# Performance work log

Hardware: AMD Instinct MI355X
Metric: run time of the kernel (lower is better)

## Reference

```python
import jax, jax.numpy as jnp
import numpy as np

P = 16       # n_partitions
E = 512      # entity_dim
H = 512      # hidden_dim
N = 8192     # number of entities in the batch


def setup_inputs() -> dict:
    key = jax.random.key(0)
    ks = jax.random.split(key, 7)
    s_in = 1.0 / np.sqrt(E)
    s_h = 1.0 / np.sqrt(H)
    return {
        "e_embedding": jax.random.normal(ks[0], (N, E), dtype=jnp.float32),
        # stacked weights for the P independent SimpleMLPs (fused as batched GEMMs)
        "W0": jax.random.uniform(ks[1], (P, E, H), jnp.float32, -s_in, s_in),
        "b0": jax.random.uniform(ks[2], (P, H), jnp.float32, -s_in, s_in),
        "W1": jax.random.uniform(ks[3], (P, H, H), jnp.float32, -s_h, s_h),
        "b1": jax.random.uniform(ks[4], (P, H), jnp.float32, -s_h, s_h),
        "W2": jax.random.uniform(ks[5], (P, H, 1), jnp.float32, -s_h, s_h),
        "b2": jax.random.uniform(ks[6], (P, 1), jnp.float32, -s_h, s_h),
    }


def reference(e_embedding, W0, b0, W1, b1, W2, b2):
    # Each partition p runs SimpleMLP_p(e_embedding); fused as batched einsums.
    h = jax.nn.relu(jnp.einsum("ne,peh->pnh", e_embedding, W0) + b0[:, None, :])  # [P,N,H]
    h = jax.nn.relu(jnp.einsum("pnh,phk->pnk", h, W1) + b1[:, None, :])           # [P,N,H]
    out = jnp.einsum("pnh,pho->pno", h, W2) + b2[:, None, :]                      # [P,N,1]
    out = jax.nn.sigmoid(out)  # regularizer: fuzzy membership in [0,1]
    # torch.stack(...).squeeze().T  ->  [P,N] -> [N,P]
    return jnp.squeeze(out, axis=-1).T
```

## Files before the change

kernel.cpp:

```cpp
#include <hip/hip_runtime.h>
#include <stdint.h>

typedef _Float16 f16;
typedef _Float16 f16x8 __attribute__((ext_vector_type(8)));
typedef float floatx4 __attribute__((ext_vector_type(4)));
typedef unsigned short u16;

#define PDIM 16

__device__ __forceinline__ floatx4 mfma_16x16x32(f16x8 a, f16x8 b, floatx4 c) {
  return __builtin_amdgcn_mfma_f32_16x16x32_f16(a, b, c, 0, 0, 0);
}

__device__ __forceinline__ void stage16(const f16* g, f16* lds_base) {
  __builtin_amdgcn_global_load_lds(
      (const __attribute__((address_space(1))) void*)g,
      (__attribute__((address_space(3))) void*)lds_base, 16, 0, 0);
}

#define WAITVM4() asm volatile("s_waitcnt vmcnt(4)" ::: "memory")
#define WAITVM2() asm volatile("s_waitcnt vmcnt(2)" ::: "memory")
#define WAITVM0() asm volatile("s_waitcnt vmcnt(0)" ::: "memory")
#define BAR()     asm volatile("s_barrier" ::: "memory")
#define LGKM0()   asm volatile("s_waitcnt lgkmcnt(0)" ::: "memory")
#define SCHEDFENCE() __builtin_amdgcn_sched_barrier(0)
#define PRIO1() __builtin_amdgcn_s_setprio(1)
#define PRIO0() __builtin_amdgcn_s_setprio(0)


__device__ __forceinline__ void decode_block2(int b, int nwg, int& p, int& ht,
                                              int& nt) {
  const int NT = nwg >> 5;
  if ((NT & 7) == 0) {
    const int x  = b & 7;
    const int u  = b >> 3;
    const int i  = u & 31;
    const int cg = u >> 5;
    ht = i & 1;
    const int pl  = (i >> 1) & 1;
    const int ntl = i >> 2;
    p  = x * 2 + pl;
    nt = cg * 8 + ntl;
  } else {
    p  = b & 15;
    ht = (b >> 4) & 1;
    nt = b >> 5;
  }
}

__global__ __launch_bounds__(256) void kprep(const float* __restrict__ emb,
                                             const float* __restrict__ W0,
                                             const float* __restrict__ W1,
                                             const float* __restrict__ b0,
                                             const float* __restrict__ b1,
                                             const float* __restrict__ W2,
                                             const float* __restrict__ b2,
                                             f16* __restrict__ embB,
                                             f16* __restrict__ W0T,
                                             f16* __restrict__ W1T,
                                             float* __restrict__ smallF,
                                             int n8, int nConvBlk) {
  __shared__ unsigned int tile[16384];
  const int b = blockIdx.x;
  const int t = threadIdx.x;
  if (b < 256) {
    const int m  = b >> 7;
    const int p  = (b >> 3) & 15;
    const int tc = b & 7;
    const int hb = tc * 64;
    const float* src = (m ? W1 : W0) + ((size_t)p << 18);
    f16*         dst = (m ? W1T : W0T) + ((size_t)p << 18);
    const int er = t >> 2;
    const int hq = t & 3;
#pragma unroll
    for (int j = 0; j < 8; ++j) {
      const int e   = er + j * 64;
      const int swz = (e >> 3) & 31;
      const float* rp = src + (size_t)e * 512 + hb;
#pragma unroll
      for (int i = 0; i < 4; ++i) {
        const int hc = hq * 4 + i * 16;
        float4 v = *(const float4*)(rp + hc);
        union { f16 h2[2]; unsigned int u; } w0, w1;
        w0.h2[0] = (f16)v.x; w0.h2[1] = (f16)v.y;
        w1.h2[0] = (f16)v.z; w1.h2[1] = (f16)v.w;
        const int hp = hc >> 1;
        tile[e * 32 + (hp ^ swz)]       = w0.u;
        tile[e * 32 + ((hp + 1) ^ swz)] = w1.u;
      }
    }
    __syncthreads();
    const int w = t >> 6, l = t & 63;
#pragma unroll
    for (int P = 0; P < 16; ++P) {
      const int hl  = P * 4 + w;
      const int hp  = hl >> 1;
      const int sub = hl & 1;
      union { u16 uu[8]; uint4 v; } o;
#pragma unroll
      for (int j = 0; j < 8; ++j) {
        const int e = l * 8 + j;
        const unsigned int word = tile[e * 32 + (hp ^ ((e >> 3) & 31))];
        o.uu[j] = (u16)(sub ? (word >> 16) : (word & 0xffffu));
      }
      *(uint4*)(dst + (size_t)(hb + hl) * 512 + l * 8) = o.v;
    }
  } else if (b < 256 + nConvBlk) {
    const int i = (b - 256) * 256 + t;
    if (i < n8) {
      const float4* s = (const float4*)emb;
      float4 a = s[i * 2], bb = s[i * 2 + 1];
      union { f16 h[8]; uint4 v; } o;
      o.h[0] = (f16)a.x;  o.h[1] = (f16)a.y;  o.h[2] = (f16)a.z;  o.h[3] = (f16)a.w;
      o.h[4] = (f16)bb.x; o.h[5] = (f16)bb.y; o.h[6] = (f16)bb.z; o.h[7] = (f16)bb.w;
      *(uint4*)(embB + (size_t)i * 8) = o.v;
    }
  } else {
    const int j = (b - 256 - nConvBlk) * 256 + t;
    if (j < 24592) {
      const float* src;
      int off;
      if (j < 8192)       { src = b0; off = j; }
      else if (j < 16384) { src = b1; off = j - 8192; }
      else if (j < 24576) { src = W2; off = j - 16384; }
      else                { src = b2; off = j - 24576; }
      smallF[j] = src[off];
    }
  }
}

__device__ __forceinline__ void stageU(const f16* M, int h, int tt, f16* buf,
                                       int w, int srow8, int kg8) {
  stage16(M + (size_t)(h * 128 + w * 8 + srow8) * 512 + tt * 64 + kg8,
          buf + (w * 8) * 64);
  stage16(M + (size_t)(h * 128 + 64 + w * 8 + srow8) * 512 + tt * 64 + kg8,
          buf + (64 + w * 8) * 64);
}

__device__ __forceinline__ void gemm_core4(const f16* __restrict__ Arow,
                                           const f16* __restrict__ Brow,
                                           f16* smem, floatx4 (*acc)[2][2][4],
                                           int w, int lane) {
  const int q   = lane >> 4;
  const int mm  = lane & 15;
  const int mm7 = mm & 7;
  const int qwr = (w & 3) * 32;
  const int qwc = (w >> 2) * 64;
  const int srow8 = lane >> 3;
  const int kg8   = (((lane & 7) ^ ((lane >> 3) & 7)) * 8);

  stageU(Arow, 0, 0, smem + 0 * 8192, w, srow8, kg8);
  stageU(Brow, 0, 0, smem + 32768 + 0 * 8192, w, srow8, kg8);
  stageU(Brow, 1, 0, smem + 32768 + 1 * 8192, w, srow8, kg8);
  stageU(Arow, 1, 0, smem + 1 * 8192, w, srow8, kg8);

  f16x8 af[2][2], bv[4][2];

  for (int t = 0; t < 8; ++t) {
    const int cb = t & 1;
    const f16* Ah0 = smem + (cb * 2 + 0) * 8192;
    const f16* Ah1 = smem + (cb * 2 + 1) * 8192;
    const f16* Bh0 = smem + 32768 + (cb * 2 + 0) * 8192;
    const f16* Bh1 = smem + 32768 + (cb * 2 + 1) * 8192;
    const int nb = cb ^ 1;
    f16* nAh0 = smem + (nb * 2 + 0) * 8192;
    f16* nAh1 = smem + (nb * 2 + 1) * 8192;
    f16* nBh0 = smem + 32768 + (nb * 2 + 0) * 8192;
    f16* nBh1 = smem + 32768 + (nb * 2 + 1) * 8192;

    WAITVM4();
    BAR();
#pragma unroll
    for (int rt = 0; rt < 2; ++rt)
#pragma unroll
      for (int ks = 0; ks < 2; ++ks)
        af[rt][ks] = *(const f16x8*)&Ah0[(qwr + rt * 16 + mm) * 64 +
                                         (((ks * 4 + q) ^ mm7)) * 8];
#pragma unroll
    for (int ct = 0; ct < 4; ++ct)
#pragma unroll
      for (int ks = 0; ks < 2; ++ks)
        bv[ct][ks] = *(const f16x8*)&Bh0[(qwc + ct * 16 + mm) * 64 +
                                         (((ks * 4 + q) ^ mm7)) * 8];
    if (t < 7) stageU(Arow, 0, t + 1, nAh0, w, srow8, kg8);
    LGKM0();
    PRIO1();
#pragma unroll
    for (int rt = 0; rt < 2; ++rt)
#pragma unroll
      for (int ct = 0; ct < 4; ++ct)
#pragma unroll
        for (int ks = 0; ks < 2; ++ks)
          acc[0][0][rt][ct] = mfma_16x16x32(af[rt][ks], bv[ct][ks],
                                            acc[0][0][rt][ct]);
    PRIO0();
    SCHEDFENCE();

    if (t < 7) { WAITVM4(); } else { WAITVM2(); }
    BAR();
#pragma unroll
    for (int ct = 0; ct < 4; ++ct)
#pragma unroll
      for (int ks = 0; ks < 2; ++ks)
        bv[ct][ks] = *(const f16x8*)&Bh1[(qwc + ct * 16 + mm) * 64 +
                                         (((ks * 4 + q) ^ mm7)) * 8];
    if (t < 7) stageU(Brow, 0, t + 1, nBh0, w, srow8, kg8);
    LGKM0();
    PRIO1();
#pragma unroll
    for (int rt = 0; rt < 2; ++rt)
#pragma unroll
      for (int ct = 0; ct < 4; ++ct)
#pragma unroll
        for (int ks = 0; ks < 2; ++ks)
          acc[0][1][rt][ct] = mfma_16x16x32(af[rt][ks], bv[ct][ks],
                                            acc[0][1][rt][ct]);
    PRIO0();
    SCHEDFENCE();

    if (t < 7) { WAITVM4(); } else { WAITVM0(); }
    BAR();
#pragma unroll
    for (int rt = 0; rt < 2; ++rt)
#pragma unroll
      for (int ks = 0; ks < 2; ++ks)
        af[rt][ks] = *(const f16x8*)&Ah1[(qwr + rt * 16 + mm) * 64 +
                                         (((ks * 4 + q) ^ mm7)) * 8];
    if (t < 7) stageU(Brow, 1, t + 1, nBh1, w, srow8, kg8);
    LGKM0();
    PRIO1();
#pragma unroll
    for (int rt = 0; rt < 2; ++rt)
#pragma unroll
      for (int ct = 0; ct < 4; ++ct)
#pragma unroll
        for (int ks = 0; ks < 2; ++ks)
          acc[1][1][rt][ct] = mfma_16x16x32(af[rt][ks], bv[ct][ks],
                                            acc[1][1][rt][ct]);
    PRIO0();
    SCHEDFENCE();

    BAR();
#pragma unroll
    for (int ct = 0; ct < 4; ++ct)
#pragma unroll
      for (int ks = 0; ks < 2; ++ks)
        bv[ct][ks] = *(const f16x8*)&Bh0[(qwc + ct * 16 + mm) * 64 +
                                         (((ks * 4 + q) ^ mm7)) * 8];
    if (t < 7) stageU(Arow, 1, t + 1, nAh1, w, srow8, kg8);
    LGKM0();
    PRIO1();
#pragma unroll
    for (int rt = 0; rt < 2; ++rt)
#pragma unroll
      for (int ct = 0; ct < 4; ++ct)
#pragma unroll
        for (int ks = 0; ks < 2; ++ks)
          acc[1][0][rt][ct] = mfma_16x16x32(af[rt][ks], bv[ct][ks],
                                            acc[1][0][rt][ct]);
    PRIO0();
    SCHEDFENCE();
  }
}

__device__ __forceinline__ void gemm_core2(const f16* __restrict__ Arow,
                                           const f16* __restrict__ Brow,
                                           f16* smem, floatx4 (*acc)[2][2][4],
                                           int w, int lane) {
  const int q   = lane >> 4;
  const int mm  = lane & 15;
  const int mm7 = mm & 7;
  const int qwr = (w & 3) * 32;
  const int qwc = (w >> 2) * 64;
  const int srow8 = lane >> 3;
  const int kg8   = (((lane & 7) ^ ((lane >> 3) & 7)) * 8);

  stageU(Arow, 0, 0, smem + 0 * 8192, w, srow8, kg8);
  stageU(Brow, 0, 0, smem + 32768 + 0 * 8192, w, srow8, kg8);
  stageU(Brow, 1, 0, smem + 32768 + 1 * 8192, w, srow8, kg8);
  stageU(Arow, 1, 0, smem + 1 * 8192, w, srow8, kg8);

  f16x8 af[2][2], bv[4][2];

  for (int t = 0; t < 8; ++t) {
    const int cb = t & 1;
    const f16* Ah0 = smem + (cb * 2 + 0) * 8192;
    const f16* Ah1 = smem + (cb * 2 + 1) * 8192;
    const f16* Bh0 = smem + 32768 + (cb * 2 + 0) * 8192;
    const f16* Bh1 = smem + 32768 + (cb * 2 + 1) * 8192;
    const int nb = cb ^ 1;
    f16* nAh0 = smem + (nb * 2 + 0) * 8192;
    f16* nAh1 = smem + (nb * 2 + 1) * 8192;
    f16* nBh0 = smem + 32768 + (nb * 2 + 0) * 8192;
    f16* nBh1 = smem + 32768 + (nb * 2 + 1) * 8192;

    WAITVM4();
    SCHEDFENCE();
    BAR();
#pragma unroll
    for (int rt = 0; rt < 2; ++rt)
#pragma unroll
      for (int ks = 0; ks < 2; ++ks)
        af[rt][ks] = *(const f16x8*)&Ah0[(qwr + rt * 16 + mm) * 64 +
                                         (((ks * 4 + q) ^ mm7)) * 8];
#pragma unroll
    for (int ct = 0; ct < 4; ++ct)
#pragma unroll
      for (int ks = 0; ks < 2; ++ks)
        bv[ct][ks] = *(const f16x8*)&Bh0[(qwc + ct * 16 + mm) * 64 +
                                         (((ks * 4 + q) ^ mm7)) * 8];
    if (t < 7) {
      stageU(Arow, 0, t + 1, nAh0, w, srow8, kg8);
      stageU(Brow, 0, t + 1, nBh0, w, srow8, kg8);
    }
    PRIO1();
#pragma unroll
    for (int rt = 0; rt < 2; ++rt)
#pragma unroll
      for (int ct = 0; ct < 4; ++ct)
#pragma unroll
        for (int ks = 0; ks < 2; ++ks)
          acc[0][0][rt][ct] = mfma_16x16x32(af[rt][ks], bv[ct][ks],
                                            acc[0][0][rt][ct]);
    PRIO0();

    if (t < 7) { WAITVM4(); } else { WAITVM0(); }
    SCHEDFENCE();
    BAR();
#pragma unroll
    for (int ct = 0; ct < 4; ++ct)
#pragma unroll
      for (int ks = 0; ks < 2; ++ks)
        bv[ct][ks] = *(const f16x8*)&Bh1[(qwc + ct * 16 + mm) * 64 +
                                         (((ks * 4 + q) ^ mm7)) * 8];
    if (t < 7) {
      stageU(Brow, 1, t + 1, nBh1, w, srow8, kg8);
      stageU(Arow, 1, t + 1, nAh1, w, srow8, kg8);
    }
    PRIO1();
#pragma unroll
    for (int rt = 0; rt < 2; ++rt)
#pragma unroll
      for (int ct = 0; ct < 4; ++ct)
#pragma unroll
        for (int ks = 0; ks < 2; ++ks)
          acc[0][1][rt][ct] = mfma_16x16x32(af[rt][ks], bv[ct][ks],
                                            acc[0][1][rt][ct]);
    PRIO0();
#pragma unroll
    for (int rt = 0; rt < 2; ++rt)
#pragma unroll
      for (int ks = 0; ks < 2; ++ks)
        af[rt][ks] = *(const f16x8*)&Ah1[(qwr + rt * 16 + mm) * 64 +
                                         (((ks * 4 + q) ^ mm7)) * 8];
    PRIO1();
#pragma unroll
    for (int rt = 0; rt < 2; ++rt)
#pragma unroll
      for (int ct = 0; ct < 4; ++ct)
#pragma unroll
        for (int ks = 0; ks < 2; ++ks)
          acc[1][1][rt][ct] = mfma_16x16x32(af[rt][ks], bv[ct][ks],
                                            acc[1][1][rt][ct]);
    PRIO0();
#pragma unroll
    for (int ct = 0; ct < 4; ++ct)
#pragma unroll
      for (int ks = 0; ks < 2; ++ks)
        bv[ct][ks] = *(const f16x8*)&Bh0[(qwc + ct * 16 + mm) * 64 +
                                         (((ks * 4 + q) ^ mm7)) * 8];
    PRIO1();
#pragma unroll
    for (int rt = 0; rt < 2; ++rt)
#pragma unroll
      for (int ct = 0; ct < 4; ++ct)
#pragma unroll
        for (int ks = 0; ks < 2; ++ks)
          acc[1][0][rt][ct] = mfma_16x16x32(af[rt][ks], bv[ct][ks],
                                            acc[1][0][rt][ct]);
    PRIO0();
    SCHEDFENCE();
  }
}

__global__ __launch_bounds__(512) void kgemm1(const f16* __restrict__ emb,
                                              const f16* __restrict__ W0T,
                                              const float* __restrict__ small,
                                              f16* __restrict__ h0,
                                              int Nc) {
  __shared__ f16 smem[65536];
  const int b  = blockIdx.x;
  const int p  = b & 15;
  const int ht = (b >> 4) & 1;
  const int nt = b >> 5;
  const int n0 = nt * 256;
  const int hc0 = ht * 256;
  const int tid = threadIdx.x;
  const int w = tid >> 6;
  const int lane = tid & 63;
  const int q = lane >> 4;
  const int mm = lane & 15;

  const f16* Arow = emb + (size_t)n0 * 512;
  const f16* Brow = W0T + ((size_t)p << 18) + (size_t)hc0 * 512;

  floatx4 acc[2][2][2][4];
#pragma unroll
  for (int i = 0; i < 2; ++i)
#pragma unroll
    for (int j = 0; j < 2; ++j)
#pragma unroll
      for (int k = 0; k < 2; ++k)
#pragma unroll
        for (int l = 0; l < 4; ++l) acc[i][j][k][l] = floatx4{0.f, 0.f, 0.f, 0.f};

  gemm_core4(Arow, Brow, smem, acc, w, lane);

  __syncthreads();
  f16* Cst = smem;
#pragma unroll
  for (int P = 0; P < 4; ++P) {
    if (((w & 3) >> 1) == (P & 1)) {
#pragma unroll
      for (int qn = 0; qn < 2; ++qn)
#pragma unroll
        for (int ct = 0; ct < 4; ++ct) {
          const int col = qn * 128 + (w >> 2) * 64 + ct * 16 + mm;
          const float bvv = small[p * 512 + hc0 + col];
#pragma unroll
          for (int rt = 0; rt < 2; ++rt)
#pragma unroll
            for (int r = 0; r < 4; ++r) {
              float v = acc[P >> 1][qn][rt][ct][r] + bvv;
              v = v > 0.f ? v : 0.f;
              Cst[((w & 1) * 32 + rt * 16 + q * 4 + r) * 264 + col] = (f16)v;
            }
        }
    }
    __syncthreads();
#pragma unroll
    for (int k = 0; k < 4; ++k) {
      const int idx = tid + k * 512;
      const int row = idx >> 5;
      const int ch  = idx & 31;
      uint4 v = *(const uint4*)&Cst[row * 264 + ch * 8];
      *(uint4*)&h0[((size_t)p * Nc + n0 + P * 64 + row) * 512 + hc0 + ch * 8] = v;
    }
    if (P < 3) __syncthreads();
  }
}

__global__ __launch_bounds__(512) void kgemm2(const f16* __restrict__ h0,
                                              const f16* __restrict__ W1T,
                                              const float* __restrict__ small,
                                              float* __restrict__ pacc,
                                              int Nc) {
  __shared__ f16 smem[65536];
  __shared__ float oacc[256];
  int p, ht, nt;
  decode_block2(blockIdx.x, gridDim.x, p, ht, nt);
  const int n0 = nt * 256;
  const int hc0 = ht * 256;
  const int tid = threadIdx.x;
  const int w = tid >> 6;
  const int lane = tid & 63;
  const int q = lane >> 4;
  const int mm = lane & 15;
  if (tid < 256) oacc[tid] = 0.f;

  const f16* Arow = h0 + ((size_t)p * Nc + n0) * 512;
  const f16* Brow = W1T + ((size_t)p << 18) + (size_t)hc0 * 512;

  floatx4 acc[2][2][2][4];
#pragma unroll
  for (int i = 0; i < 2; ++i)
#pragma unroll
    for (int j = 0; j < 2; ++j)
#pragma unroll
      for (int k = 0; k < 2; ++k)
#pragma unroll
        for (int l = 0; l < 4; ++l) acc[i][j][k][l] = floatx4{0.f, 0.f, 0.f, 0.f};

  gemm_core2(Arow, Brow, smem, acc, w, lane);

  __syncthreads();
#pragma unroll
  for (int qm = 0; qm < 2; ++qm) {
    float pd[2][4];
#pragma unroll
    for (int rt = 0; rt < 2; ++rt)
#pragma unroll
      for (int r = 0; r < 4; ++r) pd[rt][r] = 0.f;
#pragma unroll
    for (int qn = 0; qn < 2; ++qn)
#pragma unroll
      for (int ct = 0; ct < 4; ++ct) {
        const int col = hc0 + qn * 128 + (w >> 2) * 64 + ct * 16 + mm;
        const float b1v = small[8192 + p * 512 + col];
        const float w2v = small[16384 + p * 512 + col];
#pragma unroll
        for (int rt = 0; rt < 2; ++rt)
#pragma unroll
          for (int r = 0; r < 4; ++r) {
            float v = acc[qm][qn][rt][ct][r] + b1v;
            v = v > 0.f ? v : 0.f;
            pd[rt][r] += v * w2v;
          }
      }
#pragma unroll
    for (int rt = 0; rt < 2; ++rt)
#pragma unroll
      for (int r = 0; r < 4; ++r) {
        float v = pd[rt][r];
        v += __shfl_xor(v, 1, 16);
        v += __shfl_xor(v, 2, 16);
        v += __shfl_xor(v, 4, 16);
        v += __shfl_xor(v, 8, 16);
        if (mm == 0)
          atomicAdd(&oacc[qm * 128 + (w & 3) * 32 + rt * 16 + q * 4 + r], v);
      }
  }
  __syncthreads();
  if (tid < 256)
    pacc[(size_t)(p * 2 + ht) * Nc + n0 + tid] = oacc[tid];
}

__global__ __launch_bounds__(256) void kfin(const float* __restrict__ pacc,
                                            const float* __restrict__ small,
                                            float* __restrict__ out, int Nc) {
  const int idx = blockIdx.x * 256 + threadIdx.x;
  if (idx >= Nc * 16) return;
  const int n = idx >> 4;
  const int p = idx & 15;
  float v = small[24576 + p];
#pragma unroll
  for (int ht = 0; ht < 2; ++ht) v += pacc[(size_t)(p * 2 + ht) * Nc + n];
  out[(size_t)n * 16 + p] = 1.f / (1.f + expf(-v));
}

__global__ __launch_bounds__(64) void knaive(const float* __restrict__ emb,
                                             const float* __restrict__ W0,
                                             const float* __restrict__ b0,
                                             const float* __restrict__ W1,
                                             const float* __restrict__ b1,
                                             const float* __restrict__ W2,
                                             const float* __restrict__ b2,
                                             float* __restrict__ out) {
  const int n = blockIdx.x >> 4;
  const int p = blockIdx.x & 15;
  __shared__ float h0s[512];
  __shared__ float h1s[512];
  const size_t wb = (size_t)p << 18;
  const int t = threadIdx.x;
  for (int h = t; h < 512; h += 64) {
    float a = 0.f;
    for (int e = 0; e < 512; ++e)
      a += emb[(size_t)n * 512 + e] * W0[wb + (size_t)e * 512 + h];
    a += b0[p * 512 + h];
    h0s[h] = a > 0.f ? a : 0.f;
  }
  __syncthreads();
  for (int k = t; k < 512; k += 64) {
    float a = 0.f;
    for (int hh = 0; hh < 512; ++hh)
      a += h0s[hh] * W1[wb + (size_t)hh * 512 + k];
    a += b1[p * 512 + k];
    h1s[k] = a > 0.f ? a : 0.f;
  }
  __syncthreads();
  float s = 0.f;
  for (int k = t; k < 512; k += 64) s += h1s[k] * W2[p * 512 + k];
  for (int off = 32; off; off >>= 1) s += __shfl_down(s, off, 64);
  if (t == 0)
    out[(size_t)n * 16 + p] = 1.f / (1.f + expf(-(s + b2[p])));
}

extern "C" void kernel_launch(void* const* d_in, const int* in_sizes, int n_in,
                              void* d_out, int out_size, void* d_ws, size_t ws_size,
                              hipStream_t stream) {
  (void)n_in; (void)out_size;
  const float* emb = (const float*)d_in[0];
  const float* W0  = (const float*)d_in[1];
  const float* b0  = (const float*)d_in[2];
  const float* W1  = (const float*)d_in[3];
  const float* b1  = (const float*)d_in[4];
  const float* W2  = (const float*)d_in[5];
  const float* b2  = (const float*)d_in[6];
  float* out = (float*)d_out;

  const int N = in_sizes[0] / 512;

  char* ws = (char*)d_ws;
  f16*   W0T    = (f16*)ws;
  f16*   W1T    = (f16*)(ws + (8ll << 20));
  float* smallF = (float*)(ws + (16ll << 20));
  float* pacc   = (float*)(ws + (16ll << 20) + 131072);
  f16*   embB   = (f16*)(ws + (16ll << 20) + 131072 + (size_t)N * 256);
  f16*   h0     = (f16*)(ws + (16ll << 20) + 131072 + (size_t)N * 256 +
                         (size_t)N * 1024);
  const long long fixed = (16ll << 20) + 131072 + (long long)N * 256 +
                          (long long)N * 1024;
  long long avail = (long long)ws_size - fixed;
  long long rows = avail > 0 ? avail / (16 * 512 * 2) : 0;
  int Nc = (int)((rows / 256) * 256);
  if (Nc > N) Nc = N;

  if (Nc < 256 || (N % 256) != 0) {
    knaive<<<dim3(N * PDIM), dim3(64), 0, stream>>>(emb, W0, b0, W1, b1, W2,
                                                    b2, out);
    return;
  }

  const int n8 = N * 512 / 8;
  const int nConvBlk = (n8 + 255) / 256;
  kprep<<<dim3(256 + nConvBlk + 97), dim3(256), 0, stream>>>(
      emb, W0, W1, b0, b1, W2, b2, embB, W0T, W1T, smallF, n8, nConvBlk);

  for (int noff = 0; noff < N; noff += Nc) {
    const int cur = (N - noff < Nc) ? (N - noff) : Nc;
    kgemm1<<<dim3(32 * (cur / 256)), dim3(512), 0, stream>>>(
        embB + (size_t)noff * 512, W0T, smallF, h0, cur);
    kgemm2<<<dim3(32 * (cur / 256)), dim3(512), 0, stream>>>(
        h0, W1T, smallF, pacc, cur);
    kfin<<<dim3((cur * 16 + 255) / 256), dim3(256), 0, stream>>>(
        pacc, smallF, out + (size_t)noff * 16, cur);
  }
}
```

Measured before the change: 245.5 us.

## Fuse final sigmoid into kgemm2 by looping both hidden halves per block

kgemm2 now handles both 256-column halves of the hidden dimension in a sequential loop inside one block, accumulating the W2 dot product in shared memory, then adds b2, applies the sigmoid and writes the output directly. This removes the kfin kernel launch and the pacc round trip through global memory. In exchange the kgemm2 grid is halved (16 blocks per 256-row tile instead of 32), so there is less parallelism and each block runs twice as long. The A tile is re-staged for each half.

```diff
diff --git a/kernel.cpp b/kernel.cpp
--- a/kernel.cpp
+++ b/kernel.cpp
@@ -27,26 +27,6 @@
 #define PRIO1() __builtin_amdgcn_s_setprio(1)
 #define PRIO0() __builtin_amdgcn_s_setprio(0)
 
-
-__device__ __forceinline__ void decode_block2(int b, int nwg, int& p, int& ht,
-                                              int& nt) {
-  const int NT = nwg >> 5;
-  if ((NT & 7) == 0) {
-    const int x  = b & 7;
-    const int u  = b >> 3;
-    const int i  = u & 31;
-    const int cg = u >> 5;
-    ht = i & 1;
-    const int pl  = (i >> 1) & 1;
-    const int ntl = i >> 2;
-    p  = x * 2 + pl;
-    nt = cg * 8 + ntl;
-  } else {
-    p  = b & 15;
-    ht = (b >> 4) & 1;
-    nt = b >> 5;
-  }
-}
 
 __global__ __launch_bounds__(256) void kprep(const float* __restrict__ emb,
                                              const float* __restrict__ W0,
@@ -263,126 +243,6 @@
   }
 }
 
-__device__ __forceinline__ void gemm_core2(const f16* __restrict__ Arow,
-                                           const f16* __restrict__ Brow,
-                                           f16* smem, floatx4 (*acc)[2][2][4],
-                                           int w, int lane) {
-  const int q   = lane >> 4;
-  const int mm  = lane & 15;
-  const int mm7 = mm & 7;
-  const int qwr = (w & 3) * 32;
-  const int qwc = (w >> 2) * 64;
-  const int srow8 = lane >> 3;
-  const int kg8   = (((lane & 7) ^ ((lane >> 3) & 7)) * 8);
-
-  stageU(Arow, 0, 0, smem + 0 * 8192, w, srow8, kg8);
-  stageU(Brow, 0, 0, smem + 32768 + 0 * 8192, w, srow8, kg8);
-  stageU(Brow, 1, 0, smem + 32768 + 1 * 8192, w, srow8, kg8);
-  stageU(Arow, 1, 0, smem + 1 * 8192, w, srow8, kg8);
-
-  f16x8 af[2][2], bv[4][2];
-
-  for (int t = 0; t < 8; ++t) {
-    const int cb = t & 1;
-    const f16* Ah0 = smem + (cb * 2 + 0) * 8192;
-    const f16* Ah1 = smem + (cb * 2 + 1) * 8192;
-    const f16* Bh0 = smem + 32768 + (cb * 2 + 0) * 8192;
-    const f16* Bh1 = smem + 32768 + (cb * 2 + 1) * 8192;
-    const int nb = cb ^ 1;
-    f16* nAh0 = smem + (nb * 2 + 0) * 8192;
-    f16* nAh1 = smem + (nb * 2 + 1) * 8192;
-    f16* nBh0 = smem + 32768 + (nb * 2 + 0) * 8192;
-    f16* nBh1 = smem + 32768 + (nb * 2 + 1) * 8192;
-
-    WAITVM4();
-    SCHEDFENCE();
-    BAR();
-#pragma unroll
-    for (int rt = 0; rt < 2; ++rt)
-#pragma unroll
-      for (int ks = 0; ks < 2; ++ks)
-        af[rt][ks] = *(const f16x8*)&Ah0[(qwr + rt * 16 + mm) * 64 +
-                                         (((ks * 4 + q) ^ mm7)) * 8];
-#pragma unroll
-    for (int ct = 0; ct < 4; ++ct)
-#pragma unroll
-      for (int ks = 0; ks < 2; ++ks)
-        bv[ct][ks] = *(const f16x8*)&Bh0[(qwc + ct * 16 + mm) * 64 +
-                                         (((ks * 4 + q) ^ mm7)) * 8];
-    if (t < 7) {
-      stageU(Arow, 0, t + 1, nAh0, w, srow8, kg8);
-      stageU(Brow, 0, t + 1, nBh0, w, srow8, kg8);
-    }
-    PRIO1();
-#pragma unroll
-    for (int rt = 0; rt < 2; ++rt)
-#pragma unroll
-      for (int ct = 0; ct < 4; ++ct)
-#pragma unroll
-        for (int ks = 0; ks < 2; ++ks)
-          acc[0][0][rt][ct] = mfma_16x16x32(af[rt][ks], bv[ct][ks],
-                                            acc[0][0][rt][ct]);
-    PRIO0();
-
-    if (t < 7) { WAITVM4(); } else { WAITVM0(); }
-    SCHEDFENCE();
-    BAR();
-#pragma unroll
-    for (int ct = 0; ct < 4; ++ct)
-#pragma unroll
-      for (int ks = 0; ks < 2; ++ks)
-        bv[ct][ks] = *(const f16x8*)&Bh1[(qwc + ct * 16 + mm) * 64 +
-                                         (((ks * 4 + q) ^ mm7)) * 8];
-    if (t < 7) {
-      stageU(Brow, 1, t + 1, nBh1, w, srow8, kg8);
-      stageU(Arow, 1, t + 1, nAh1, w, srow8, kg8);
-    }
-    PRIO1();
-#pragma unroll
-    for (int rt = 0; rt < 2; ++rt)
-#pragma unroll
-      for (int ct = 0; ct < 4; ++ct)
-#pragma unroll
-        for (int ks = 0; ks < 2; ++ks)
-          acc[0][1][rt][ct] = mfma_16x16x32(af[rt][ks], bv[ct][ks],
-                                            acc[0][1][rt][ct]);
-    PRIO0();
-#pragma unroll
-    for (int rt = 0; rt < 2; ++rt)
-#pragma unroll
-      for (int ks = 0; ks < 2; ++ks)
-        af[rt][ks] = *(const f16x8*)&Ah1[(qwr + rt * 16 + mm) * 64 +
-                                         (((ks * 4 + q) ^ mm7)) * 8];
-    PRIO1();
-#pragma unroll
-    for (int rt = 0; rt < 2; ++rt)
-#pragma unroll
-      for (int ct = 0; ct < 4; ++ct)
-#pragma unroll
-        for (int ks = 0; ks < 2; ++ks)
-          acc[1][1][rt][ct] = mfma_16x16x32(af[rt][ks], bv[ct][ks],
-                                            acc[1][1][rt][ct]);
-    PRIO0();
-#pragma unroll
-    for (int ct = 0; ct < 4; ++ct)
-#pragma unroll
-      for (int ks = 0; ks < 2; ++ks)
-        bv[ct][ks] = *(const f16x8*)&Bh0[(qwc + ct * 16 + mm) * 64 +
-                                         (((ks * 4 + q) ^ mm7)) * 8];
-    PRIO1();
-#pragma unroll
-    for (int rt = 0; rt < 2; ++rt)
-#pragma unroll
-      for (int ct = 0; ct < 4; ++ct)
-#pragma unroll
-        for (int ks = 0; ks < 2; ++ks)
-          acc[1][0][rt][ct] = mfma_16x16x32(af[rt][ks], bv[ct][ks],
-                                            acc[1][0][rt][ct]);
-    PRIO0();
-    SCHEDFENCE();
-  }
-}
-
 __global__ __launch_bounds__(512) void kgemm1(const f16* __restrict__ emb,
                                               const f16* __restrict__ W0T,
                                               const float* __restrict__ small,
@@ -450,17 +310,153 @@
   }
 }
 
+__device__ __forceinline__ void gemm_core2(const f16* __restrict__ Arow,
+                                           const f16* __restrict__ Brow,
+                                           f16* smem, floatx4 (*acc)[2][2][4],
+                                           int w, int lane) {
+  const int q   = lane >> 4;
+  const int mm  = lane & 15;
+  const int mm7 = mm & 7;
+  const int qwr = (w & 3) * 32;
+  const int qwc = (w >> 2) * 64;
+  const int srow8 = lane >> 3;
+  const int kg8   = (((lane & 7) ^ ((lane >> 3) & 7)) * 8);
+
+  stageU(Arow, 0, 0, smem + 0 * 8192, w, srow8, kg8);
+  stageU(Brow, 0, 0, smem + 32768 + 0 * 8192, w, srow8, kg8);
+  stageU(Brow, 1, 0, smem + 32768 + 1 * 8192, w, srow8, kg8);
+  stageU(Arow, 1, 0, smem + 1 * 8192, w, srow8, kg8);
+
+  f16x8 af[2][2], bv[4][2];
+
+  for (int t = 0; t < 8; ++t) {
+    const int cb = t & 1;
+    const f16* Ah0 = smem + (cb * 2 + 0) * 8192;
+    const f16* Ah1 = smem + (cb * 2 + 1) * 8192;
+    const f16* Bh0 = smem + 32768 + (cb * 2 + 0) * 8192;
+    const f16* Bh1 = smem + 32768 + (cb * 2 + 1) * 8192;
+    const int nb = cb ^ 1;
+    f16* nAh0 = smem + (nb * 2 + 0) * 8192;
+    f16* nAh1 = smem + (nb * 2 + 1) * 8192;
+    f16* nBh0 = smem + 32768 + (nb * 2 + 0) * 8192;
+    f16* nBh1 = smem + 32768 + (nb * 2 + 1) * 8192;
+
+    WAITVM4();
+    SCHEDFENCE();
+    BAR();
+#pragma unroll
+    for (int rt = 0; rt < 2; ++rt)
+#pragma unroll
+      for (int ks = 0; ks < 2; ++ks)
+        af[rt][ks] = *(const f16x8*)&Ah0[(qwr + rt * 16 + mm) * 64 +
+                                         (((ks * 4 + q) ^ mm7)) * 8];
+#pragma unroll
+    for (int ct = 0; ct < 4; ++ct)
+#pragma unroll
+      for (int ks = 0; ks < 2; ++ks)
+        bv[ct][ks] = *(const f16x8*)&Bh0[(qwc + ct * 16 + mm) * 64 +
+                                         (((ks * 4 + q) ^ mm7)) * 8];
+    if (t < 7) {
+      stageU(Arow, 0, t + 1, nAh0, w, srow8, kg8);
+      stageU(Brow, 0, t + 1, nBh0, w, srow8, kg8);
+    }
+    PRIO1();
+#pragma unroll
+    for (int rt = 0; rt < 2; ++rt)
+#pragma unroll
+      for (int ct = 0; ct < 4; ++ct)
+#pragma unroll
+        for (int ks = 0; ks < 2; ++ks)
+          acc[0][0][rt][ct] = mfma_16x16x32(af[rt][ks], bv[ct][ks],
+                                            acc[0][0][rt][ct]);
+    PRIO0();
+
+    if (t < 7) { WAITVM4(); } else { WAITVM0(); }
+    SCHEDFENCE();
+    BAR();
+#pragma unroll
+    for (int ct = 0; ct < 4; ++ct)
+#pragma unroll
+      for (int ks = 0; ks < 2; ++ks)
+        bv[ct][ks] = *(const f16x8*)&Bh1[(qwc + ct * 16 + mm) * 64 +
+                                         (((ks * 4 + q) ^ mm7)) * 8];
+    if (t < 7) {
+      stageU(Brow, 1, t + 1, nBh1, w, srow8, kg8);
+      stageU(Arow, 1, t + 1, nAh1, w, srow8, kg8);
+    }
+    PRIO1();
+#pragma unroll
+    for (int rt = 0; rt < 2; ++rt)
+#pragma unroll
+      for (int ct = 0; ct < 4; ++ct)
+#pragma unroll
+        for (int ks = 0; ks < 2; ++ks)
+          acc[0][1][rt][ct] = mfma_16x16x32(af[rt][ks], bv[ct][ks],
+                                            acc[0][1][rt][ct]);
+    PRIO0();
+#pragma unroll
+    for (int rt = 0; rt < 2; ++rt)
+#pragma unroll
+      for (int ks = 0; ks < 2; ++ks)
+        af[rt][ks] = *(const f16x8*)&Ah1[(qwr + rt * 16 + mm) * 64 +
+                                         (((ks * 4 + q) ^ mm7)) * 8];
+    PRIO1();
+#pragma unroll
+    for (int rt = 0; rt < 2; ++rt)
+#pragma unroll
+      for (int ct = 0; ct < 4; ++ct)
+#pragma unroll
+        for (int ks = 0; ks < 2; ++ks)
+          acc[1][1][rt][ct] = mfma_16x16x32(af[rt][ks], bv[ct][ks],
+                                            acc[1][1][rt][ct]);
+    PRIO0();
+#pragma unroll
+    for (int ct = 0; ct < 4; ++ct)
+#pragma unroll
+      for (int ks = 0; ks < 2; ++ks)
+        bv[ct][ks] = *(const f16x8*)&Bh0[(qwc + ct * 16 + mm) * 64 +
+                                         (((ks * 4 + q) ^ mm7)) * 8];
+    PRIO1();
+#pragma unroll
+    for (int rt = 0; rt < 2; ++rt)
+#pragma unroll
+      for (int ct = 0; ct < 4; ++ct)
+#pragma unroll
+        for (int ks = 0; ks < 2; ++ks)
+          acc[1][0][rt][ct] = mfma_16x16x32(af[rt][ks], bv[ct][ks],
+                                            acc[1][0][rt][ct]);
+    PRIO0();
+    SCHEDFENCE();
+  }
+}
+
+__device__ __forceinline__ void decode_blockf(int b, int nwg, int& p, int& nt) {
+  const int NT = nwg >> 4;
+  if ((NT & 7) == 0) {
+    const int x  = b & 7;
+    const int u  = b >> 3;
+    const int i  = u & 15;
+    const int cg = u >> 4;
+    const int pl  = i & 1;
+    const int ntl = i >> 1;
+    p  = x * 2 + pl;
+    nt = cg * 8 + ntl;
+  } else {
+    p  = b & 15;
+    nt = b >> 4;
+  }
+}
+
 __global__ __launch_bounds__(512) void kgemm2(const f16* __restrict__ h0,
                                               const f16* __restrict__ W1T,
                                               const float* __restrict__ small,
-                                              float* __restrict__ pacc,
+                                              float* __restrict__ out,
                                               int Nc) {
   __shared__ f16 smem[65536];
   __shared__ float oacc[256];
-  int p, ht, nt;
-  decode_block2(blockIdx.x, gridDim.x, p, ht, nt);
+  int p, nt;
+  decode_blockf(blockIdx.x, gridDim.x, p, nt);
   const int n0 = nt * 256;
-  const int hc0 = ht * 256;
   const int tid = threadIdx.x;
   const int w = tid >> 6;
   const int lane = tid & 63;
@@ -469,73 +465,69 @@
   if (tid < 256) oacc[tid] = 0.f;
 
   const f16* Arow = h0 + ((size_t)p * Nc + n0) * 512;
-  const f16* Brow = W1T + ((size_t)p << 18) + (size_t)hc0 * 512;
-
-  floatx4 acc[2][2][2][4];
-#pragma unroll
-  for (int i = 0; i < 2; ++i)
-#pragma unroll
-    for (int j = 0; j < 2; ++j)
-#pragma unroll
-      for (int k = 0; k < 2; ++k)
-#pragma unroll
-        for (int l = 0; l < 4; ++l) acc[i][j][k][l] = floatx4{0.f, 0.f, 0.f, 0.f};
-
-  gemm_core2(Arow, Brow, smem, acc, w, lane);
-
-  __syncthreads();
-#pragma unroll
-  for (int qm = 0; qm < 2; ++qm) {
-    float pd[2][4];
-#pragma unroll
-    for (int rt = 0; rt < 2; ++rt)
-#pragma unroll
-      for (int r = 0; r < 4; ++r) pd[rt][r] = 0.f;
-#pragma unroll
-    for (int qn = 0; qn < 2; ++qn)
-#pragma unroll
-      for (int ct = 0; ct < 4; ++ct) {
-        const int col = hc0 + qn * 128 + (w >> 2) * 64 + ct * 16 + mm;
-        const float b1v = small[8192 + p * 512 + col];
-        const float w2v = small[16384 + p * 512 + col];
-#pragma unroll
-        for (int rt = 0; rt < 2; ++rt)
-#pragma unroll
-          for (int r = 0; r < 4; ++r) {
-            float v = acc[qm][qn][rt][ct][r] + b1v;
-            v = v > 0.f ? v : 0.f;
-            pd[rt][r] += v * w2v;
-          }
-      }
-#pragma unroll
-    for (int rt = 0; rt < 2; ++rt)
-#pragma unroll
-      for (int r = 0; r < 4; ++r) {
-        float v = pd[rt][r];
-        v += __shfl_xor(v, 1, 16);
-        v += __shfl_xor(v, 2, 16);
-        v += __shfl_xor(v, 4, 16);
-        v += __shfl_xor(v, 8, 16);
-        if (mm == 0)
-          atomicAdd(&oacc[qm * 128 + (w & 3) * 32 + rt * 16 + q * 4 + r], v);
-      }
-  }
-  __syncthreads();
-  if (tid < 256)
-    pacc[(size_t)(p * 2 + ht) * Nc + n0 + tid] = oacc[tid];
-}
-
-__global__ __launch_bounds__(256) void kfin(const float* __restrict__ pacc,
-                                            const float* __restrict__ small,
-                                            float* __restrict__ out, int Nc) {
-  const int idx = blockIdx.x * 256 + threadIdx.x;
-  if (idx >= Nc * 16) return;
-  const int n = idx >> 4;
-  const int p = idx & 15;
-  float v = small[24576 + p];
-#pragma unroll
-  for (int ht = 0; ht < 2; ++ht) v += pacc[(size_t)(p * 2 + ht) * Nc + n];
-  out[(size_t)n * 16 + p] = 1.f / (1.f + expf(-v));
+
+#pragma unroll 1
+  for (int ht = 0; ht < 2; ++ht) {
+    const int hc0 = ht * 256;
+    const f16* Brow = W1T + ((size_t)p << 18) + (size_t)hc0 * 512;
+
+    floatx4 acc[2][2][2][4];
+#pragma unroll
+    for (int i = 0; i < 2; ++i)
+#pragma unroll
+      for (int j = 0; j < 2; ++j)
+#pragma unroll
+        for (int k = 0; k < 2; ++k)
+#pragma unroll
+          for (int l = 0; l < 4; ++l)
+            acc[i][j][k][l] = floatx4{0.f, 0.f, 0.f, 0.f};
+
+    gemm_core2(Arow, Brow, smem, acc, w, lane);
+
+    __syncthreads();
+#pragma unroll
+    for (int qm = 0; qm < 2; ++qm) {
+      float pd[2][4];
+#pragma unroll
+      for (int rt = 0; rt < 2; ++rt)
+#pragma unroll
+        for (int r = 0; r < 4; ++r) pd[rt][r] = 0.f;
+#pragma unroll
+      for (int qn = 0; qn < 2; ++qn)
+#pragma unroll
+        for (int ct = 0; ct < 4; ++ct) {
+          const int col = hc0 + qn * 128 + (w >> 2) * 64 + ct * 16 + mm;
+          const float b1v = small[8192 + p * 512 + col];
+          const float w2v = small[16384 + p * 512 + col];
+#pragma unroll
+          for (int rt = 0; rt < 2; ++rt)
+#pragma unroll
+            for (int r = 0; r < 4; ++r) {
+              float v = acc[qm][qn][rt][ct][r] + b1v;
+              v = v > 0.f ? v : 0.f;
+              pd[rt][r] += v * w2v;
+            }
+        }
+#pragma unroll
+      for (int rt = 0; rt < 2; ++rt)
+#pragma unroll
+        for (int r = 0; r < 4; ++r) {
+          float v = pd[rt][r];
+          v += __shfl_xor(v, 1, 16);
+          v += __shfl_xor(v, 2, 16);
+          v += __shfl_xor(v, 4, 16);
+          v += __shfl_xor(v, 8, 16);
+          if (mm == 0)
+            atomicAdd(&oacc[qm * 128 + (w & 3) * 32 + rt * 16 + q * 4 + r], v);
+        }
+    }
+    __syncthreads();
+  }
+
+  if (tid < 256) {
+    const float v = oacc[tid] + small[24576 + p];
+    out[(size_t)(n0 + tid) * 16 + p] = 1.f / (1.f + expf(-v));
+  }
 }
 
 __global__ __launch_bounds__(64) void knaive(const float* __restrict__ emb,
@@ -598,6 +590,7 @@
   f16*   embB   = (f16*)(ws + (16ll << 20) + 131072 + (size_t)N * 256);
   f16*   h0     = (f16*)(ws + (16ll << 20) + 131072 + (size_t)N * 256 +
                          (size_t)N * 1024);
+  (void)pacc;
   const long long fixed = (16ll << 20) + 131072 + (long long)N * 256 +
                           (long long)N * 1024;
   long long avail = (long long)ws_size - fixed;
@@ -620,9 +613,7 @@
     const int cur = (N - noff < Nc) ? (N - noff) : Nc;
     kgemm1<<<dim3(32 * (cur / 256)), dim3(512), 0, stream>>>(
         embB + (size_t)noff * 512, W0T, smallF, h0, cur);
-    kgemm2<<<dim3(32 * (cur / 256)), dim3(512), 0, stream>>>(
-        h0, W1T, smallF, pacc, cur);
-    kfin<<<dim3((cur * 16 + 255) / 256), dim3(256), 0, stream>>>(
-        pacc, smallF, out + (size_t)noff * 16, cur);
-  }
-}
+    kgemm2<<<dim3(16 * (cur / 256)), dim3(512), 0, stream>>>(
+        h0, W1T, smallF, out + (size_t)noff * 16, cur);
+  }
+}
```

After: 259.7 us. +5.8%, slower.
